# Performance work log

Hardware: AMD Instinct MI355X
Metric: run time of the kernel (lower is better)

The kernel has to match this reference:

```python
import jax, jax.numpy as jnp
import numpy as np

D_MODEL = 256
KSIZE = 16
EPS = 1e-5


def conv1d(x, w, b):
    # x: [B, C, N], w: [O, C, K], SAME padding over node axis
    y = jax.lax.conv_general_dilated(x, w, window_strides=(1,), padding='SAME',
                                     dimension_numbers=('NCH', 'OIH', 'NCH'))
    return y + b[None, :, None]


def layernorm(x, g, b):
    mu = jnp.mean(x, axis=-1, keepdims=True)
    var = jnp.mean(jnp.square(x - mu), axis=-1, keepdims=True)
    return (x - mu) * jax.lax.rsqrt(var + EPS) * g + b


def setup_inputs() -> dict:
    key = jax.random.key(0)
    ks = jax.random.split(key, 16)
    B, N, d, K = 4, 2048, D_MODEL, KSIZE
    conv_scale = 1.0 / np.sqrt(d * K)
    lin_scale = 1.0 / np.sqrt(d)
    return {
        'src': jax.random.normal(ks[0], (B, N, d), jnp.float32),
        'x_lst': jnp.zeros((B, N, N), jnp.float32),
        'adj': jax.random.randint(ks[1], (B, N, N), 0, 2, jnp.int32),
        'dis': jax.random.uniform(ks[2], (B, N, N), jnp.float32),
        'Wq': jax.random.normal(ks[3], (d, d, K), jnp.float32) * conv_scale,
        'bq': jnp.zeros((d,), jnp.float32),
        'Wk': jax.random.normal(ks[4], (d, d, K), jnp.float32) * conv_scale,
        'bk': jnp.zeros((d,), jnp.float32),
        'Wv': jax.random.normal(ks[5], (d, d, K), jnp.float32) * conv_scale,
        'bv': jnp.zeros((d,), jnp.float32),
        'W1': jax.random.normal(ks[6], (d, d), jnp.float32) * lin_scale,
        'b1': jnp.zeros((d,), jnp.float32),
        'W2': jax.random.normal(ks[7], (d, d), jnp.float32) * lin_scale,
        'b2': jnp.zeros((d,), jnp.float32),
        'W3': jax.random.normal(ks[8], (d, d), jnp.float32) * lin_scale,
        'b3': jnp.zeros((d,), jnp.float32),
        'g1': jnp.ones((d,), jnp.float32),
        'be1': jnp.zeros((d,), jnp.float32),
        'g2': jnp.ones((d,), jnp.float32),
        'be2': jnp.zeros((d,), jnp.float32),
    }


def reference(src, x_lst, adj, dis, Wq, bq, Wk, bk, Wv, bv,
              W1, b1, W2, b2, W3, b3, g1, be1, g2, be2):
    # ---- _ga_block: transpose to channel-major, graph attention ----
    x = jnp.swapaxes(src, -2, -1)                      # [B, d, N]
    q = conv1d(x, Wq, bq)                              # [B, d, N]
    k = conv1d(x, Wk, bk)
    v = conv1d(x, Wv, bv)
    scale = 1.0 / jnp.sqrt(jnp.asarray(D_MODEL, src.dtype))
    scores = jnp.einsum('bdn,bdm->bnm', q, k) * scale  # [B, N, N]
    scores = scores - dis                              # distance bias
    scores = jnp.where(adj > 0, scores, jnp.asarray(-1e9, scores.dtype))
    attn = jax.nn.softmax(scores, axis=-1)             # [B, N, N]
    x_lst_new = x_lst + attn                           # accumulated attention state
    out = jnp.einsum('bnm,bdm->bdn', attn, v)          # [B, d, N]
    x1 = jnp.swapaxes(out, -2, -1)                     # [B, N, d] (dropout = identity in eval)
    # ---- residual + norm1 ----
    h = layernorm(src + x1, g1, be1)
    # ---- 3-layer LeakyReLU MLP + residual + norm2 ----
    m = jax.nn.leaky_relu(h @ W1.T + b1)
    m = jax.nn.leaky_relu(m @ W2.T + b2)
    m = m @ W3.T + b3
    h = layernorm(h + m, g2, be2)
    return h, x_lst_new
```

## Files before the change

kernel.cpp:

```cpp
#include <hip/hip_runtime.h>
#include <stdint.h>

typedef _Float16 h16;
typedef _Float16 h4v __attribute__((ext_vector_type(4)));
typedef _Float16 h8v __attribute__((ext_vector_type(8)));
typedef float    f4v __attribute__((ext_vector_type(4)));
typedef int      i4v __attribute__((ext_vector_type(4)));

#define NBATCH 4
#define NNODE  2048
#define DM     256
#define NPAD   2063
#define QKELEM 2097152
#define PARTN  (8192 * 256)

__device__ __forceinline__ void async16(const void* g, void* l) {
#if __has_builtin(__builtin_amdgcn_global_load_lds)
  __builtin_amdgcn_global_load_lds((__attribute__((address_space(1))) void*)g,
                                   (__attribute__((address_space(3))) void*)l, 16, 0, 0);
#else
  *(f4v*)l = *(const f4v*)g;
#endif
}

#define BARRIER() do { asm volatile("" ::: "memory"); __builtin_amdgcn_s_barrier(); asm volatile("" ::: "memory"); } while (0)
#define MFMA16 __builtin_amdgcn_mfma_f32_16x16x32_f16

__device__ __forceinline__ void gemm_tile(
    const h16* Abase, int astride,
    const h16* Bbase, int bstride,
    h16* As, h16* Bs, f4v acc[4][4], int kiters)
{
  const int tid  = threadIdx.x;
  const int lane = tid & 63;
  const int wv   = tid >> 6;
  const int srow = tid >> 2;
  const int sch  = ((tid & 3) ^ ((tid >> 3) & 3)) * 8;
  const h16* gA0 = Abase + (long)srow * astride + sch;
  const h16* gA1 = Abase + (long)(srow + 64) * astride + sch;
  const h16* gB0 = Bbase + (long)srow * bstride + sch;
  const h16* gB1 = Bbase + (long)(srow + 64) * bstride + sch;
  h16* lA0 = As + tid * 8;
  h16* lA1 = As + 2048 + tid * 8;
  h16* lB0 = Bs + tid * 8;
  h16* lB1 = Bs + 2048 + tid * 8;
  const int swz = ((lane & 15) >> 1) & 3;
  const int qq  = ((lane >> 4) ^ swz) * 8;
  const int amr = ((wv & 1) * 64 + (lane & 15)) * 32 + qq;
  const int bnr = ((wv >> 1) * 64 + (lane & 15)) * 32 + qq;

  for (int kt = 0; kt < kiters; ++kt) {
    const int k0 = kt * 32;
    __syncthreads();
    async16(gA0 + k0, lA0);
    async16(gA1 + k0, lA1);
    async16(gB0 + k0, lB0);
    async16(gB1 + k0, lB1);
    asm volatile("s_waitcnt vmcnt(0)" ::: "memory");
    __syncthreads();
    h8v af[4], bf[4];
#pragma unroll
    for (int i = 0; i < 4; ++i) af[i] = *(const h8v*)(As + amr + i * 512);
#pragma unroll
    for (int j = 0; j < 4; ++j) bf[j] = *(const h8v*)(Bs + bnr + j * 512);
#pragma unroll
    for (int i = 0; i < 4; ++i)
#pragma unroll
      for (int j = 0; j < 4; ++j)
        acc[i][j] = MFMA16(af[i], bf[j], acc[i][j], 0, 0, 0);
  }
}

__device__ __forceinline__ void zero_acc(f4v acc[4][4]) {
#pragma unroll
  for (int i = 0; i < 4; ++i)
#pragma unroll
    for (int j = 0; j < 4; ++j) {
      f4v z = {0.f, 0.f, 0.f, 0.f};
      acc[i][j] = z;
    }
}

template<int ASTRIDE, int BSTRIDE>
__device__ __forceinline__ void gemm256_pipe(
    const h16* __restrict__ Abase, const h16* __restrict__ Bbase,
    h16* As, h16* Bs, f4v (&acc)[8][4], const int kiters)
{
  const int tid  = threadIdx.x;
  const int lane = tid & 63, wv = tid >> 6;

  const int rh = tid >> 3;
  const int cs = (((tid & 7) ^ ((tid >> 3) & 7)) << 3);
  const h16* AgT = Abase + (long)rh * ASTRIDE + cs;
  const h16* BgT = Bbase + (long)rh * BSTRIDE + cs;
  h16* lA = As + tid * 8;
  h16* lB = Bs + tid * 8;

  auto stageA = [&](int kt, int half) {
    h16* d = lA + ((kt & 1) << 14) + (half << 13);
    const h16* g = AgT + (long)half * 128 * ASTRIDE + kt * 64;
    async16(g, d);
    async16(g + 64 * ASTRIDE, d + 4096);
  };
  auto stageB = [&](int kt, int half) {
    h16* d = lB + ((kt & 1) << 14) + (half << 13);
    const h16* g = BgT + (long)half * 128 * BSTRIDE + kt * 64;
    async16(g, d);
    async16(g + 64 * BSTRIDE, d + 4096);
  };

  const int wr = wv >> 2, wc = wv & 3;
  const int e0 = (((lane >> 4) ^ (lane & 7)) << 3);
  const int e1 = e0 ^ 32;
  const h16* pA0 = As + (wr * 128 + (lane & 15)) * 64 + e0;
  const h16* pA1 = pA0 + (e1 - e0);
  const h16* pB0 = Bs + (wc * 64 + (lane & 15)) * 64 + e0;
  const h16* pB1 = pB0 + (e1 - e0);

#pragma unroll
  for (int i = 0; i < 8; ++i)
#pragma unroll
    for (int j = 0; j < 4; ++j) { f4v z = {0.f, 0.f, 0.f, 0.f}; acc[i][j] = z; }

  stageA(0, 0); stageA(0, 1); stageB(0, 0); stageB(0, 1); stageA(1, 0);
  asm volatile("s_waitcnt vmcnt(2)" ::: "memory");
  BARRIER();

#pragma unroll 1
  for (int kt = 0; kt < kiters; ++kt) {
    const int sb = (kt & 1) << 14;
    h8v ar[4][2], bL[2][2], bR[2][2];
#pragma unroll
    for (int i = 0; i < 4; ++i) {
      ar[i][0] = *(const h8v*)(pA0 + sb + i * 1024);
      ar[i][1] = *(const h8v*)(pA1 + sb + i * 1024);
    }
#pragma unroll
    for (int j = 0; j < 2; ++j) {
      bL[j][0] = *(const h8v*)(pB0 + sb + j * 1024);
      bL[j][1] = *(const h8v*)(pB1 + sb + j * 1024);
    }
    if (kt < kiters - 1) stageA(kt + 1, 1);
    BARRIER();
    __builtin_amdgcn_s_setprio(1);
#pragma unroll
    for (int i = 0; i < 4; ++i)
#pragma unroll
      for (int j = 0; j < 2; ++j) {
        acc[i][j] = MFMA16(ar[i][0], bL[j][0], acc[i][j], 0, 0, 0);
        acc[i][j] = MFMA16(ar[i][1], bL[j][1], acc[i][j], 0, 0, 0);
      }
    __builtin_amdgcn_s_setprio(0);
    BARRIER();
#pragma unroll
    for (int j = 0; j < 2; ++j) {
      bR[j][0] = *(const h8v*)(pB0 + sb + (j + 2) * 1024);
      bR[j][1] = *(const h8v*)(pB1 + sb + (j + 2) * 1024);
    }
    if (kt < kiters - 1) stageB(kt + 1, 0);
    BARRIER();
    __builtin_amdgcn_s_setprio(1);
#pragma unroll
    for (int i = 0; i < 4; ++i)
#pragma unroll
      for (int j = 0; j < 2; ++j) {
        acc[i][j + 2] = MFMA16(ar[i][0], bR[j][0], acc[i][j + 2], 0, 0, 0);
        acc[i][j + 2] = MFMA16(ar[i][1], bR[j][1], acc[i][j + 2], 0, 0, 0);
      }
    __builtin_amdgcn_s_setprio(0);
    BARRIER();
#pragma unroll
    for (int i = 0; i < 4; ++i) {
      ar[i][0] = *(const h8v*)(pA0 + sb + (i + 4) * 1024);
      ar[i][1] = *(const h8v*)(pA1 + sb + (i + 4) * 1024);
    }
    if (kt < kiters - 1) stageB(kt + 1, 1);
    BARRIER();
    __builtin_amdgcn_s_setprio(1);
#pragma unroll
    for (int i = 0; i < 4; ++i)
#pragma unroll
      for (int j = 0; j < 2; ++j) {
        acc[i + 4][j + 2] = MFMA16(ar[i][0], bR[j][0], acc[i + 4][j + 2], 0, 0, 0);
        acc[i + 4][j + 2] = MFMA16(ar[i][1], bR[j][1], acc[i + 4][j + 2], 0, 0, 0);
      }
    __builtin_amdgcn_s_setprio(0);
    BARRIER();
#pragma unroll
    for (int j = 0; j < 2; ++j) {
      bL[j][0] = *(const h8v*)(pB0 + sb + j * 1024);
      bL[j][1] = *(const h8v*)(pB1 + sb + j * 1024);
    }
    if (kt < kiters - 2) {
      stageA(kt + 2, 0);
      asm volatile("s_waitcnt vmcnt(2)" ::: "memory");
    } else if (kt == kiters - 2) {
      asm volatile("s_waitcnt vmcnt(0)" ::: "memory");
    }
    BARRIER();
    __builtin_amdgcn_s_setprio(1);
#pragma unroll
    for (int i = 0; i < 4; ++i)
#pragma unroll
      for (int j = 0; j < 2; ++j) {
        acc[i + 4][j] = MFMA16(ar[i][0], bL[j][0], acc[i + 4][j], 0, 0, 0);
        acc[i + 4][j] = MFMA16(ar[i][1], bL[j][1], acc[i + 4][j], 0, 0, 0);
      }
    __builtin_amdgcn_s_setprio(0);
    BARRIER();
  }
}

#define NSRC_BLK 8252
__global__ __launch_bounds__(256) void prep_all_kernel(
    const float* __restrict__ src,
    const float* __restrict__ Wq, const float* __restrict__ Wk, const float* __restrict__ Wv,
    const float* __restrict__ W1, const float* __restrict__ W2, const float* __restrict__ W3,
    h16* __restrict__ Xpad, h16* __restrict__ Wt, h16* __restrict__ Wl)
{
  __shared__ float plds[16][257];
  const int bi = blockIdx.x, tid = threadIdx.x;
  if (bi < NSRC_BLK) {
    int idx = bi * 256 + tid;
    int c = idx & 255;
    int row = idx >> 8;
    int b = row / NPAD;
    int n = row - b * NPAD;
    float v = 0.f;
    int ns = n - 7;
    if (ns >= 0 && ns < NNODE) v = src[((long)b * NNODE + ns) * DM + c];
    Xpad[idx] = (h16)v;
  } else if (bi < NSRC_BLK + 768) {
    const int q = bi - NSRC_BLK;
    const int w = q >> 8, o = q & 255;
    const float* W = (w == 0) ? Wq : (w == 1) ? Wk : Wv;
    const float* base = W + (long)o * 4096;
    f4v r0 = *(const f4v*)(base + tid * 16);
    f4v r1 = *(const f4v*)(base + tid * 16 + 4);
    f4v r2 = *(const f4v*)(base + tid * 16 + 8);
    f4v r3 = *(const f4v*)(base + tid * 16 + 12);
#pragma unroll
    for (int k = 0; k < 4; ++k) {
      plds[k][tid] = r0[k]; plds[4 + k][tid] = r1[k];
      plds[8 + k][tid] = r2[k]; plds[12 + k][tid] = r3[k];
    }
    __syncthreads();
    const int t = tid >> 4, c0 = (tid & 15) * 16;
    h16* out = Wt + ((long)(w * 256 + o)) * 4096 + t * 256 + c0;
    h8v o0, o1;
#pragma unroll
    for (int k = 0; k < 8; ++k) { o0[k] = (h16)plds[t][c0 + k]; o1[k] = (h16)plds[t][c0 + 8 + k]; }
    *(h8v*)out = o0;
    *(h8v*)(out + 8) = o1;
  } else {
    int idx = (bi - NSRC_BLK - 768) * 256 + tid;
    int w = idx >> 16;
    int rem = idx & 65535;
    const float* W = (w == 0) ? W1 : (w == 1) ? W2 : W3;
    Wl[idx] = (h16)W[rem];
  }
}

__global__ __launch_bounds__(512) void conv_gemm256_kernel(
    const h16* __restrict__ Xpad, const h16* __restrict__ Wt,
    h16* __restrict__ Qp, h16* __restrict__ Kp, h16* __restrict__ Vp)
{
  __shared__ __align__(16) h16 As[32768];
  __shared__ __align__(16) h16 Bs[32768];
  const int lane = threadIdx.x & 63, wv = threadIdx.x >> 6;
  const int mt = blockIdx.x, w = blockIdx.y, ks = blockIdx.z;
  const int m0 = mt * 256;
  const int b  = m0 >> 11, n0 = m0 & 2047;

  const h16* Abase = Xpad + ((long)(b * NPAD + n0) << 8) + ((long)ks << 11);
  const h16* Bbase = Wt + ((long)w << 20) + ((long)ks << 11);

  f4v acc[8][4];
  gemm256_pipe<256, 4096>(Abase, Bbase, As, Bs, acc, 32);

  h16* dst = ((w == 0) ? Qp : (w == 1) ? Kp : Vp) + (long)ks * QKELEM;
  const int wr = wv >> 2, wc = wv & 3;
  const int rb = (lane >> 4) * 4;
  const int cb = wc * 64 + (lane & 15);
  const int mrow0 = m0 + wr * 128;
#pragma unroll
  for (int i = 0; i < 8; ++i)
#pragma unroll
    for (int j = 0; j < 4; ++j) {
      const int gc = cb + j * 16;
#pragma unroll
      for (int e = 0; e < 4; ++e) {
        const int gr = mrow0 + i * 16 + rb + e;
        dst[(long)gr * 256 + gc] = (h16)acc[i][j][e];
      }
    }
}

__global__ __launch_bounds__(256) void conv_reduce_kernel(
    const h16* __restrict__ Qp, const h16* __restrict__ Kp, const h16* __restrict__ Vp,
    const float* __restrict__ bq, const float* __restrict__ bk, const float* __restrict__ bv,
    h16* __restrict__ Qb, h16* __restrict__ Kb, h16* __restrict__ Vt)
{
  __shared__ float T[64][65];
  const int bi = blockIdx.x, tid = threadIdx.x;
  if (bi < 2048) {
    const long gid = (long)bi * 256 + tid;
    const int which = gid >= (QKELEM / 8);
    const long e = (gid - (long)which * (QKELEM / 8)) * 8;
    const h16* P = which ? Kp : Qp;
    const float* bias = which ? bk : bq;
    h8v p0 = *(const h8v*)(P + e);
    h8v p1 = *(const h8v*)(P + QKELEM + e);
    const int c0 = (int)(e & 255);
    h8v o;
#pragma unroll
    for (int k = 0; k < 8; ++k) o[k] = (h16)((float)p0[k] + (float)p1[k] + bias[c0 + k]);
    *(h8v*)((which ? Kb : Qb) + e) = o;
  } else {
    const int q = bi - 2048;
    const int mt = q >> 2, ct = q & 3;
    const int m0 = mt * 64, c0 = ct * 64;
    const int b = m0 >> 11, n0 = m0 & 2047;
    const int rr = tid >> 3, cc = (tid & 7) * 8;
#pragma unroll
    for (int p = 0; p < 2; ++p) {
      const int r = p * 32 + rr;
      const long so = (long)(m0 + r) * 256 + c0 + cc;
      h8v p0 = *(const h8v*)(Vp + so);
      h8v p1 = *(const h8v*)(Vp + QKELEM + so);
#pragma unroll
      for (int e = 0; e < 8; ++e) T[r][cc + e] = (float)p0[e] + (float)p1[e];
    }
    __syncthreads();
#pragma unroll
    for (int p = 0; p < 2; ++p) {
      const int d = p * 32 + rr;
      const float bias_v = bv[c0 + d];
      h8v o;
#pragma unroll
      for (int e = 0; e < 8; ++e) o[e] = (h16)(T[cc + e][d] + bias_v);
      *(h8v*)(Vt + ((long)(b * 256 + c0 + d)) * 2048 + n0 + cc) = o;
    }
  }
}

__global__ __launch_bounds__(256) void scores_gemm_kernel(
    const h16* __restrict__ Q, const h16* __restrict__ Km,
    const float* __restrict__ dis, const int* __restrict__ adj,
    h16* __restrict__ Sh)
{
  __shared__ __align__(16) h16 As[4096];
  __shared__ __align__(16) h16 Bs[4096];
  const int nt = blockIdx.x, mt = blockIdx.y, b = blockIdx.z;
  const h16* Abase = Q + ((long)b * NNODE + nt * 128) * 256;
  const h16* Bbase = Km + ((long)b * NNODE + mt * 128) * 256;
  f4v acc[4][4];
  zero_acc(acc);
  gemm_tile(Abase, 256, Bbase, 256, As, Bs, acc, 8);

  const int lane = threadIdx.x & 63, wv = threadIdx.x >> 6;
  const int rbase = (wv & 1) * 64 + (lane >> 4) * 4;
  const int cbase = (wv >> 1) * 64 + (lane & 15);
  const long base = (long)b * NNODE * NNODE;
#pragma unroll
  for (int i = 0; i < 4; ++i) {
#pragma unroll
    for (int e = 0; e < 4; ++e) {
      const long row = nt * 128 + rbase + i * 16 + e;
      const long ro = base + row * 2048 + mt * 128;
#pragma unroll
      for (int j = 0; j < 4; ++j) {
        const int col = cbase + j * 16;
        const int a = adj[ro + col];
        const float dd = dis[ro + col];
        const float sv = acc[i][j][e] * 0.0625f - dd;
        Sh[ro + col] = (a > 0) ? (h16)sv : (h16)(-30000.0f);
      }
    }
  }
}

__global__ __launch_bounds__(256) void softmax_kernel(
    h16* __restrict__ Sh, const float* __restrict__ x_lst, float* __restrict__ out_x)
{
  const int r = blockIdx.x;
  const long ro = (long)r * 2048;
  const int tid = threadIdx.x, lane = tid & 63, wv = tid >> 6;
  const int j0 = tid * 4;
  __shared__ float wmax[4], wsum[4];

  h4v sv0 = *(const h4v*)(Sh + ro + j0);
  h4v sv1 = *(const h4v*)(Sh + ro + 1024 + j0);

  float s[8];
#pragma unroll
  for (int k = 0; k < 4; ++k) { s[k] = (float)sv0[k]; s[k + 4] = (float)sv1[k]; }

  float m = s[0];
#pragma unroll
  for (int k = 1; k < 8; ++k) m = fmaxf(m, s[k]);
#pragma unroll
  for (int off = 32; off > 0; off >>= 1) m = fmaxf(m, __shfl_xor(m, off, 64));
  if (lane == 0) wmax[wv] = m;
  __syncthreads();
  m = fmaxf(fmaxf(wmax[0], wmax[1]), fmaxf(wmax[2], wmax[3]));

  float p[8], ls = 0.f;
#pragma unroll
  for (int k = 0; k < 8; ++k) { p[k] = __expf(s[k] - m); ls += p[k]; }
#pragma unroll
  for (int off = 32; off > 0; off >>= 1) ls += __shfl_xor(ls, off, 64);
  if (lane == 0) wsum[wv] = ls;
  __syncthreads();
  const float inv = 1.0f / (wsum[0] + wsum[1] + wsum[2] + wsum[3]);

  f4v x0 = *(const f4v*)(x_lst + ro + j0);
  f4v x1 = *(const f4v*)(x_lst + ro + 1024 + j0);
  f4v o0, o1;
  h4v pv0, pv1;
#pragma unroll
  for (int k = 0; k < 4; ++k) {
    const float a = p[k] * inv, bq = p[k + 4] * inv;
    o0[k] = x0[k] + a; o1[k] = x1[k] + bq;
    pv0[k] = (h16)a; pv1[k] = (h16)bq;
  }
  *(f4v*)(out_x + ro + j0) = o0;
  *(f4v*)(out_x + ro + 1024 + j0) = o1;
  *(h4v*)(Sh + ro + j0) = pv0;
  *(h4v*)(Sh + ro + 1024 + j0) = pv1;
}

__global__ __launch_bounds__(256) void av_gemm_kernel(
    const h16* __restrict__ Attn, const h16* __restrict__ Vt, h16* __restrict__ X1p)
{
  __shared__ __align__(16) h16 As[4096];
  __shared__ __align__(16) h16 Bs[4096];
  const int nt = blockIdx.x, b = blockIdx.z;
  const int ct = blockIdx.y & 1, ks = blockIdx.y >> 1;
  const h16* Abase = Attn + ((long)b * NNODE + nt * 128) * 2048 + ks * 1024;
  const h16* Bbase = Vt + ((long)b * 256 + ct * 128) * 2048 + ks * 1024;
  f4v acc[4][4];
  zero_acc(acc);
  gemm_tile(Abase, 2048, Bbase, 2048, As, Bs, acc, 32);

  const int lane = threadIdx.x & 63, wv = threadIdx.x >> 6;
  const int rbase = (wv & 1) * 64 + (lane >> 4) * 4;
  const int cbase = (wv >> 1) * 64 + (lane & 15);
  h16* dst = X1p + (long)ks * PARTN;
#pragma unroll
  for (int i = 0; i < 4; ++i) {
#pragma unroll
    for (int e = 0; e < 4; ++e) {
      const long row = (long)b * NNODE + nt * 128 + rbase + i * 16 + e;
#pragma unroll
      for (int j = 0; j < 4; ++j) {
        const int col = ct * 128 + cbase + j * 16;
        dst[row * 256 + col] = (h16)acc[i][j][e];
      }
    }
  }
}

__device__ __forceinline__ float wred_sum(float v) {
#pragma unroll
  for (int off = 32; off > 0; off >>= 1) v += __shfl_xor(v, off, 64);
  return v;
}

__global__ __launch_bounds__(256) void ln1_kernel(
    const float* __restrict__ X, const h16* __restrict__ Y, const h16* __restrict__ Y2,
    const float* __restrict__ g, const float* __restrict__ bb,
    float* __restrict__ outF, h16* __restrict__ outH)
{
  const int wv = threadIdx.x >> 6, lane = threadIdx.x & 63;
  const long r = (long)blockIdx.x * 4 + wv;
  const long off = r * 256 + lane * 4;
  f4v x = *(const f4v*)(X + off);
  h4v y = *(const h4v*)(Y + off);
  h4v y2 = *(const h4v*)(Y2 + off);
  float v[4];
  float sum = 0.f, sq = 0.f;
#pragma unroll
  for (int k = 0; k < 4; ++k) {
    v[k] = x[k] + (float)y[k] + (float)y2[k];
    sum += v[k]; sq += v[k] * v[k];
  }
  sum = wred_sum(sum);
  sq  = wred_sum(sq);
  const float mu = sum * (1.0f / 256.0f);
  const float var = sq * (1.0f / 256.0f) - mu * mu;
  const float rs = rsqrtf(var + 1e-5f);
  f4v gg = *(const f4v*)(g + lane * 4);
  f4v be = *(const f4v*)(bb + lane * 4);
  f4v o;
#pragma unroll
  for (int k = 0; k < 4; ++k) o[k] = (v[k] - mu) * rs * gg[k] + be[k];
  *(f4v*)(outF + off) = o;
  h4v hv;
#pragma unroll
  for (int k = 0; k < 4; ++k) hv[k] = (h16)o[k];
  *(h4v*)(outH + off) = hv;
}

__global__ __launch_bounds__(256) void mlp_fused_kernel(
    const h16* __restrict__ H16, const float* __restrict__ Hf,
    const h16* __restrict__ Wl,
    const float* __restrict__ b1, const float* __restrict__ b2, const float* __restrict__ b3,
    const float* __restrict__ g2, const float* __restrict__ be2,
    float* __restrict__ out_h)
{
  __shared__ h16 Xa[32][264];
  __shared__ h16 Xb[32][264];
  __shared__ __align__(16) h16 Bs[8192];
  const int tid = threadIdx.x, lane = tid & 63, wv = tid >> 6;
  const int m0 = blockIdx.x * 32;

  {
    const int r = tid >> 3, cq = (tid & 7) * 32;
    const h16* s = H16 + (long)(m0 + r) * 256 + cq;
#pragma unroll
    for (int k = 0; k < 4; ++k)
      *(h8v*)&Xa[r][cq + k * 8] = *(const h8v*)(s + k * 8);
  }

  const int srow = tid >> 2;
  const int sch  = ((tid & 3) ^ ((tid >> 3) & 3)) * 8;
  h16* lB = Bs + tid * 8;
  const int quad = lane >> 4;
  const float* biases[3] = {b1, b2, b3};

  for (int layer = 0; layer < 3; ++layer) {
    const h16* W = Wl + layer * 65536;
    const h16 (*Xi)[264] = (layer == 1) ? (const h16(*)[264])Xb : (const h16(*)[264])Xa;
    h16 (*Xo)[264] = (layer == 1) ? Xa : Xb;
    f4v acc[2][4];
#pragma unroll
    for (int i = 0; i < 2; ++i)
#pragma unroll
      for (int j = 0; j < 4; ++j) { f4v z = {0.f,0.f,0.f,0.f}; acc[i][j] = z; }

    for (int kt = 0; kt < 8; ++kt) {
      __syncthreads();
      const h16* gB = W + (long)srow * 256 + kt * 32 + sch;
      async16(gB, lB);
      async16(gB + 64 * 256, lB + 64 * 32);
      async16(gB + 128 * 256, lB + 128 * 32);
      async16(gB + 192 * 256, lB + 192 * 32);
      asm volatile("s_waitcnt vmcnt(0)" ::: "memory");
      __syncthreads();
      h8v af[2], bf[4];
#pragma unroll
      for (int i = 0; i < 2; ++i)
        af[i] = *(const h8v*)&Xi[i * 16 + (lane & 15)][kt * 32 + quad * 8];
#pragma unroll
      for (int j = 0; j < 4; ++j) {
        const int n = wv * 64 + j * 16 + (lane & 15);
        const int q = (quad ^ ((n >> 1) & 3)) * 8;
        bf[j] = *(const h8v*)(Bs + n * 32 + q);
      }
#pragma unroll
      for (int i = 0; i < 2; ++i)
#pragma unroll
        for (int j = 0; j < 4; ++j)
          acc[i][j] = MFMA16(af[i], bf[j], acc[i][j], 0, 0, 0);
    }
    const int rb = quad * 4;
    const int cb = wv * 64 + (lane & 15);
    const float* bias = biases[layer];
    const bool leaky = (layer < 2);
#pragma unroll
    for (int j = 0; j < 4; ++j) {
      const int col = cb + j * 16;
      const float bv = bias[col];
#pragma unroll
      for (int i = 0; i < 2; ++i)
#pragma unroll
        for (int e = 0; e < 4; ++e) {
          float v = acc[i][j][e] + bv;
          if (leaky) v = (v >= 0.f) ? v : 0.01f * v;
          Xo[i * 16 + rb + e][col] = (h16)v;
        }
    }
  }
  __syncthreads();

  const int r = tid >> 3, c0 = (tid & 7) * 32;
  const float* hrow = Hf + (long)(m0 + r) * 256 + c0;
  float v[32];
  float s = 0.f, sq = 0.f;
#pragma unroll
  for (int k8 = 0; k8 < 8; ++k8) {
    f4v h4 = *(const f4v*)(hrow + k8 * 4);
#pragma unroll
    for (int e = 0; e < 4; ++e) {
      float t = (float)Xb[r][c0 + k8 * 4 + e] + h4[e];
      v[k8 * 4 + e] = t; s += t; sq += t * t;
    }
  }
#pragma unroll
  for (int off = 1; off < 8; off <<= 1) { s += __shfl_xor(s, off, 64); sq += __shfl_xor(sq, off, 64); }
  const float mu = s * (1.0f / 256.0f);
  const float var = sq * (1.0f / 256.0f) - mu * mu;
  const float rs = rsqrtf(var + 1e-5f);
  float* orow = out_h + (long)(m0 + r) * 256 + c0;
#pragma unroll
  for (int k8 = 0; k8 < 8; ++k8) {
    f4v gg = *(const f4v*)(g2 + c0 + k8 * 4);
    f4v be = *(const f4v*)(be2 + c0 + k8 * 4);
    f4v o;
#pragma unroll
    for (int e = 0; e < 4; ++e) o[e] = (v[k8 * 4 + e] - mu) * rs * gg[e] + be[e];
    *(f4v*)(orow + k8 * 4) = o;
  }
}

extern "C" void kernel_launch(void* const* d_in, const int* in_sizes, int n_in,
                              void* d_out, int out_size, void* d_ws, size_t ws_size,
                              hipStream_t stream)
{
  const float* src  = (const float*)d_in[0];
  const float* xlst = (const float*)d_in[1];
  const int*   adj  = (const int*)d_in[2];
  const float* dis  = (const float*)d_in[3];
  const float* Wq   = (const float*)d_in[4];
  const float* bq   = (const float*)d_in[5];
  const float* Wk   = (const float*)d_in[6];
  const float* bk   = (const float*)d_in[7];
  const float* Wv   = (const float*)d_in[8];
  const float* bvp  = (const float*)d_in[9];
  const float* W1   = (const float*)d_in[10];
  const float* b1   = (const float*)d_in[11];
  const float* W2   = (const float*)d_in[12];
  const float* b2   = (const float*)d_in[13];
  const float* W3   = (const float*)d_in[14];
  const float* b3   = (const float*)d_in[15];
  const float* g1   = (const float*)d_in[16];
  const float* be1  = (const float*)d_in[17];
  const float* g2   = (const float*)d_in[18];
  const float* be2  = (const float*)d_in[19];
  (void)in_sizes; (void)n_in; (void)out_size; (void)ws_size;

  char* ws = (char*)d_ws;
  size_t off = 0;
  auto alloc = [&](size_t bytes) -> void* {
    void* p = ws + off;
    off += (bytes + 1023) & ~(size_t)1023;
    return p;
  };
  h16*   Xpad = (h16*)  alloc((size_t)NBATCH * NPAD * DM * 2);
  h16*   Wt   = (h16*)  alloc((size_t)3 * 256 * 4096 * 2);
  h16*   Wl   = (h16*)  alloc((size_t)3 * 256 * 256 * 2);
  h16*   Qb   = (h16*)  alloc((size_t)QKELEM * 2);
  h16*   Kb   = (h16*)  alloc((size_t)QKELEM * 2);
  h16*   Vt   = (h16*)  alloc((size_t)QKELEM * 2);
  char*  R    = (char*) alloc((size_t)66000 * 1024);
  h16*   Qp   = (h16*)R;
  h16*   Kp   = (h16*)(R + (size_t)2 * QKELEM * 2);
  h16*   Vp   = (h16*)(R + (size_t)4 * QKELEM * 2);
  h16*   Sh   = (h16*)R;
  h16*   X1p  = (h16*)(R + (size_t)8 * QKELEM * 2);
  float* H    = (float*)(R + (size_t)12 * QKELEM * 2);
  h16*   H16  = (h16*)((char*)H + (size_t)PARTN * 4);

  float* out_h = (float*)d_out;
  float* out_x = out_h + (size_t)NBATCH * NNODE * DM;

  prep_all_kernel<<<NSRC_BLK + 768 + 768, 256, 0, stream>>>(
      src, Wq, Wk, Wv, W1, W2, W3, Xpad, Wt, Wl);
  conv_gemm256_kernel<<<dim3(32, 3, 2), 512, 0, stream>>>(Xpad, Wt, Qp, Kp, Vp);
  conv_reduce_kernel<<<2048 + 512, 256, 0, stream>>>(
      Qp, Kp, Vp, bq, bk, bvp, Qb, Kb, Vt);
  scores_gemm_kernel<<<dim3(16, 16, 4), 256, 0, stream>>>(Qb, Kb, dis, adj, Sh);
  softmax_kernel<<<NBATCH * NNODE, 256, 0, stream>>>(Sh, xlst, out_x);
  av_gemm_kernel<<<dim3(16, 4, 4), 256, 0, stream>>>(Sh, Vt, X1p);
  ln1_kernel<<<(NBATCH * NNODE) / 4, 256, 0, stream>>>(src, X1p, X1p + PARTN, g1, be1, H, H16);
  mlp_fused_kernel<<<NBATCH * NNODE / 32, 256, 0, stream>>>(
      H16, H, Wl, b1, b2, b3, g2, be2, out_h);
}
```

Measured before the change: 421.4 us.

## Stream dis/adj mask into LDS during the score GEMM k-loop

The score GEMM kernel now loads the distance and adjacency tiles with coalesced 16-byte vector loads inside the k-loop, spread over the eight k-steps. It folds them into a half-precision additive bias in a padded LDS buffer, so the epilogue reads the bias from LDS instead of doing strided scalar global loads of adj and dis. The aim is to hide the dominant N×N input traffic behind the MFMA work and to coalesce it. In exchange it adds about 36 KB of LDS, which may reduce occupancy. Storing -dis in fp16 before adding it to the score also changes rounding slightly.

```diff
diff --git a/kernel.cpp b/kernel.cpp
--- a/kernel.cpp
+++ b/kernel.cpp
@@ -344,6 +344,7 @@
   }
 }
 
+#define MBS 144
 __global__ __launch_bounds__(256) void scores_gemm_kernel(
     const h16* __restrict__ Q, const h16* __restrict__ Km,
     const float* __restrict__ dis, const int* __restrict__ adj,
@@ -351,30 +352,85 @@
 {
   __shared__ __align__(16) h16 As[4096];
   __shared__ __align__(16) h16 Bs[4096];
+  __shared__ __align__(16) h16 Mb[128 * MBS];
   const int nt = blockIdx.x, mt = blockIdx.y, b = blockIdx.z;
+  const int tid = threadIdx.x, lane = tid & 63, wv = tid >> 6;
+
   const h16* Abase = Q + ((long)b * NNODE + nt * 128) * 256;
   const h16* Bbase = Km + ((long)b * NNODE + mt * 128) * 256;
+
+  const int srow = tid >> 2;
+  const int sch  = ((tid & 3) ^ ((tid >> 3) & 3)) * 8;
+  const h16* gA0 = Abase + (long)srow * 256 + sch;
+  const h16* gA1 = Abase + (long)(srow + 64) * 256 + sch;
+  const h16* gB0 = Bbase + (long)srow * 256 + sch;
+  const h16* gB1 = Bbase + (long)(srow + 64) * 256 + sch;
+  h16* lA0 = As + tid * 8;
+  h16* lA1 = As + 2048 + tid * 8;
+  h16* lB0 = Bs + tid * 8;
+  h16* lB1 = Bs + 2048 + tid * 8;
+  const int swz = ((lane & 15) >> 1) & 3;
+  const int qq  = ((lane >> 4) ^ swz) * 8;
+  const int amr = ((wv & 1) * 64 + (lane & 15)) * 32 + qq;
+  const int bnr = ((wv >> 1) * 64 + (lane & 15)) * 32 + qq;
+
+  const long gbase = (long)b * NNODE * NNODE + (long)(nt * 128) * 2048 + mt * 128;
   f4v acc[4][4];
   zero_acc(acc);
-  gemm_tile(Abase, 256, Bbase, 256, As, Bs, acc, 8);
-
-  const int lane = threadIdx.x & 63, wv = threadIdx.x >> 6;
+
+#pragma unroll 1
+  for (int kt = 0; kt < 8; ++kt) {
+    const int f0 = kt * 2048 + tid * 4;
+    const int f1 = f0 + 1024;
+    const int r0 = f0 >> 7, c0 = f0 & 127;
+    const int r1 = f1 >> 7, c1 = f1 & 127;
+    const long g0 = gbase + (long)r0 * 2048 + c0;
+    const long g1 = gbase + (long)r1 * 2048 + c1;
+    __syncthreads();
+    f4v dv0 = *(const f4v*)(dis + g0);
+    f4v dv1 = *(const f4v*)(dis + g1);
+    i4v av0 = *(const i4v*)(adj + g0);
+    i4v av1 = *(const i4v*)(adj + g1);
+    const int k0 = kt * 32;
+    async16(gA0 + k0, lA0);
+    async16(gA1 + k0, lA1);
+    async16(gB0 + k0, lB0);
+    async16(gB1 + k0, lB1);
+    asm volatile("s_waitcnt vmcnt(0)" ::: "memory");
+    h4v m0, m1;
+#pragma unroll
+    for (int k = 0; k < 4; ++k) {
+      m0[k] = (av0[k] > 0) ? (h16)(-dv0[k]) : (h16)(-30000.0f);
+      m1[k] = (av1[k] > 0) ? (h16)(-dv1[k]) : (h16)(-30000.0f);
+    }
+    *(h4v*)(Mb + r0 * MBS + c0) = m0;
+    *(h4v*)(Mb + r1 * MBS + c1) = m1;
+    __syncthreads();
+    h8v af[4], bf[4];
+#pragma unroll
+    for (int i = 0; i < 4; ++i) af[i] = *(const h8v*)(As + amr + i * 512);
+#pragma unroll
+    for (int j = 0; j < 4; ++j) bf[j] = *(const h8v*)(Bs + bnr + j * 512);
+#pragma unroll
+    for (int i = 0; i < 4; ++i)
+#pragma unroll
+      for (int j = 0; j < 4; ++j)
+        acc[i][j] = MFMA16(af[i], bf[j], acc[i][j], 0, 0, 0);
+  }
+
   const int rbase = (wv & 1) * 64 + (lane >> 4) * 4;
   const int cbase = (wv >> 1) * 64 + (lane & 15);
-  const long base = (long)b * NNODE * NNODE;
 #pragma unroll
   for (int i = 0; i < 4; ++i) {
 #pragma unroll
     for (int e = 0; e < 4; ++e) {
-      const long row = nt * 128 + rbase + i * 16 + e;
-      const long ro = base + row * 2048 + mt * 128;
+      const int row = rbase + i * 16 + e;
+      const long ro = gbase + (long)row * 2048;
 #pragma unroll
       for (int j = 0; j < 4; ++j) {
         const int col = cbase + j * 16;
-        const int a = adj[ro + col];
-        const float dd = dis[ro + col];
-        const float sv = acc[i][j][e] * 0.0625f - dd;
-        Sh[ro + col] = (a > 0) ? (h16)sv : (h16)(-30000.0f);
+        const float sv = acc[i][j][e] * 0.0625f + (float)Mb[row * MBS + col];
+        Sh[ro + col] = (h16)sv;
       }
     }
   }
```

Result: faster. 413.1 us (-2.0%).
